# Optimization experiments

Measured on AMD Instinct MI355X. Metric: run time of the kernel, lower is better.

## Reference

```python
import jax, jax.numpy as jnp
import numpy as np

EPS = 1e-5
KH = KW = 3
PAD = 1

def conv3x3(x, w, b=None):
    out = jax.lax.conv_general_dilated(
        x, w, window_strides=(1, 1), padding=((PAD, PAD), (PAD, PAD)),
        dimension_numbers=("NCHW", "OIHW", "NCHW"))
    if b is not None:
        out = out + b[None, :, None, None]
    return out

def batchnorm(x, gamma, beta):
    # training-mode BatchNorm2d: batch statistics over (N, H, W)
    mean = x.mean(axis=(0, 2, 3), keepdims=True)
    var = x.var(axis=(0, 2, 3), keepdims=True)
    return gamma[None, :, None, None] * (x - mean) / jnp.sqrt(var + EPS) + beta[None, :, None, None]

def bilinear_gather(x, y_pos, x_pos):
    # x: [B,C,H,W]; y_pos/x_pos: [B,P,H,W] (P = KH*KW sampling taps)
    # zero padding outside image (mmcv modulated deform conv semantics)
    B, C, H, W = x.shape
    P = y_pos.shape[1]
    x_flat = x.reshape(B, C, H * W)
    y0 = jnp.floor(y_pos)
    x0 = jnp.floor(x_pos)
    ly = y_pos - y0
    lx = x_pos - x0
    out = jnp.zeros((B, C, P, H, W), dtype=x.dtype)
    for dy, dx, wgt in ((0, 0, (1 - ly) * (1 - lx)), (0, 1, (1 - ly) * lx),
                        (1, 0, ly * (1 - lx)), (1, 1, ly * lx)):
        yi = y0 + dy
        xi = x0 + dx
        valid = ((yi >= 0) & (yi <= H - 1) & (xi >= 0) & (xi <= W - 1)).astype(x.dtype)
        yc = jnp.clip(yi, 0, H - 1).astype(jnp.int32)
        xc = jnp.clip(xi, 0, W - 1).astype(jnp.int32)
        idx = (yc * W + xc).reshape(B, 1, P * H * W)
        vals = jnp.take_along_axis(x_flat, jnp.broadcast_to(idx, (B, C, P * H * W)), axis=2)
        vals = vals.reshape(B, C, P, H, W)
        out = out + vals * (wgt * valid)[:, None]
    return out  # [B,C,P,H,W]

def modulated_deform_conv(x, w_off, b_off, w_dcn):
    B, C, H, W = x.shape
    P = KH * KW
    off = conv3x3(x, w_off, b_off)  # [B, 3*P, H, W]
    o1, o2, m = jnp.split(off, 3, axis=1)
    offset = jnp.concatenate([o1, o2], axis=1)            # [B, 2P, H, W]
    offset = offset.reshape(B, P, 2, H, W)                # channel 2p -> dy, 2p+1 -> dx
    mask = jax.nn.sigmoid(m)                              # [B, P, H, W]
    hh = jnp.arange(H, dtype=x.dtype)
    ww = jnp.arange(W, dtype=x.dtype)
    ky = jnp.arange(KH, dtype=x.dtype)
    kx = jnp.arange(KW, dtype=x.dtype)
    # base sampling grid per tap p = ky*KW + kx: (h - PAD + ky, w - PAD + kx)
    base_y = (hh[None, :] - PAD + ky[:, None])            # [KH, H]
    base_x = (ww[None, :] - PAD + kx[:, None])            # [KW, W]
    base_y = jnp.broadcast_to(base_y[:, None, :, None], (KH, KW, H, W)).reshape(P, H, W)
    base_x = jnp.broadcast_to(base_x[None, :, None, :], (KH, KW, H, W)).reshape(P, H, W)
    y_pos = base_y[None] + offset[:, :, 0]                # [B,P,H,W]
    x_pos = base_x[None] + offset[:, :, 1]
    sampled = bilinear_gather(x, y_pos, x_pos)            # [B,C,P,H,W]
    sampled = sampled * mask[:, None]
    w = w_dcn.reshape(w_dcn.shape[0], C, P)               # [O, C, P]
    return jnp.einsum("bcphw,ocp->bohw", sampled, w)

def setup_inputs() -> dict:
    key = jax.random.key(0)
    ks = jax.random.split(key, 10)
    B, Ch, H, W = 4, 256, 64, 64
    Cin, Cout = 2 * Ch, 256
    P = KH * KW
    inp = {
        "input_v": jax.random.normal(ks[0], (B, Ch, H, W), jnp.float32),
        "input_i": jax.random.normal(ks[1], (B, Ch, H, W), jnp.float32),
        "w_off": jax.random.normal(ks[2], (3 * P, Cin, KH, KW), jnp.float32) * 0.01,
        "b_off": jnp.zeros((3 * P,), jnp.float32),
        "w_dcn": jax.random.normal(ks[3], (Cout, Cin, KH, KW), jnp.float32) * (1.0 / np.sqrt(Cin * P)),
        "gamma1": jnp.ones((Cout,), jnp.float32),
        "beta1": jnp.zeros((Cout,), jnp.float32),
        "w2": jax.random.normal(ks[4], (Cout, Cout, KH, KW), jnp.float32) * (1.0 / np.sqrt(Cout * P)),
        "gamma2": jnp.ones((Cout,), jnp.float32),
        "beta2": jnp.zeros((Cout,), jnp.float32),
    }
    return inp

def reference(input_v, input_i, w_off, b_off, w_dcn, gamma1, beta1, w2, gamma2, beta2):
    x = jnp.concatenate([input_v, input_i], axis=1)
    out = modulated_deform_conv(x, w_off, b_off, w_dcn)
    out = jax.nn.relu(batchnorm(out, gamma1, beta1))
    out = jax.nn.relu(batchnorm(conv3x3(out, w2), gamma2, beta2))
    return out
```

## Files before the change

### kernel.cpp

```cpp
#include <hip/hip_runtime.h>
#include <cstdint>
#include <cstddef>

typedef unsigned short u16;
typedef __attribute__((ext_vector_type(8))) short s16x8;
typedef __attribute__((ext_vector_type(4))) float f32x4;

#define DEV __device__ __forceinline__

DEV float bf2f(short u){
  union { unsigned int i; float f; } v;
  v.i = ((unsigned int)(u16)u) << 16;
  return v.f;
}
DEV short f2bf(float f){
  union { float f; unsigned int i; } v; v.f = f;
  unsigned int u = v.i;
  u += 0x7fffu + ((u >> 16) & 1u);
  return (short)(u >> 16);
}
DEV s16x8 s16x8_zero(){
  s16x8 z;
#pragma unroll
  for(int j=0;j<8;j++) z[j]=0;
  return z;
}
DEV f32x4 f32x4_zero(){
  f32x4 z;
#pragma unroll
  for(int j=0;j<4;j++) z[j]=0.f;
  return z;
}
DEV f32x4 mfma16(s16x8 a, s16x8 b, f32x4 c){
  return __builtin_amdgcn_mfma_f32_16x16x32_bf16(a, b, c, 0, 0, 0);
}
DEV void bar_lds(){
  asm volatile("s_waitcnt lgkmcnt(0)");
  __builtin_amdgcn_s_barrier();
}

static constexpr size_t OFF_ACC_B  = 0;
static constexpr size_t OUT1_ACC_B = 2097152;
static constexpr size_t OUT2_ACC_B = OUT1_ACC_B + 16777216;
static constexpr size_t STATS_B    = OUT2_ACC_B + 16777216;
static constexpr size_t ZERO_BYTES = STATS_B + 4096;
static constexpr size_t XN_B       = ZERO_BYTES;
static constexpr size_t OUT1N_B    = XN_B + 16777216;
static constexpr size_t WOFFT_B    = OUT1N_B + 8388608;
static constexpr size_t WDCNT_B    = WOFFT_B + 294912;
static constexpr size_t W2T_B      = WDCNT_B + 2359296;

__global__ void k_x_to_nhwc(const float* __restrict__ v, const float* __restrict__ vi,
                            u16* __restrict__ xn){
  __shared__ float tile[64][65];
  const int b = blockIdx.z, c0 = blockIdx.y*64, hw0 = blockIdx.x*64;
  const float* src = (c0 < 256) ? (v  + ((size_t)b*256 + c0)      *4096)
                                : (vi + ((size_t)b*256 + (c0-256))*4096);
  const int t = threadIdx.x;
#pragma unroll
  for(int k=0;k<16;k++){
    int idx = t + k*256;
    int cl = idx >> 6, wl = idx & 63;
    tile[cl][wl] = src[(size_t)cl*4096 + hw0 + wl];
  }
  __syncthreads();
#pragma unroll
  for(int k=0;k<16;k++){
    int idx = t + k*256;
    int wl = idx >> 6, cl = idx & 63;
    xn[(size_t)(b*4096 + hw0 + wl)*512 + c0 + cl] = (u16)f2bf(tile[cl][wl]);
  }
}

__global__ void k_prep_woff(const float* __restrict__ w, u16* __restrict__ wt){
  int idx = blockIdx.x*256 + threadIdx.x;
  if(idx >= 32*4608) return;
  int n = idx / 4608, k = idx % 4608;
  int t = k >> 9, c = k & 511;
  float val = (n < 27) ? w[(size_t)(n*512 + c)*9 + t] : 0.f;
  wt[idx] = (u16)f2bf(val);
}
__global__ void k_prep_wdcn(const float* __restrict__ w, u16* __restrict__ wt){
  int idx = blockIdx.x*256 + threadIdx.x;
  if(idx >= 256*4608) return;
  int n = idx / 4608, k = idx % 4608;
  int t = k >> 9, c = k & 511;
  wt[idx] = (u16)f2bf(w[(size_t)(n*512 + c)*9 + t]);
}
__global__ void k_prep_w2(const float* __restrict__ w, u16* __restrict__ wt){
  int idx = blockIdx.x*256 + threadIdx.x;
  if(idx >= 256*2304) return;
  int n = idx / 2304, k = idx % 2304;
  int t = k >> 8, c = k & 255;
  wt[idx] = (u16)f2bf(w[(size_t)(n*256 + c)*9 + t]);
}

__global__ __launch_bounds__(256, 2) void k_conv_off(
    const u16* __restrict__ xn, const u16* __restrict__ wt, float* __restrict__ offa){
  __shared__ short A_lds[4][128][8];
  __shared__ short B_lds[4][32][8];
  const int tid = threadIdx.x;
  const int lane = tid & 63, wid = tid >> 6;
  const int quad = lane >> 4, ln = lane & 15;
  const int m0 = blockIdx.x * 128;
  const int b = m0 >> 12;
  const int h0 = (m0 & 4095) >> 6;
  const int ks = blockIdx.y;
  const int ts0 = (ks == 3) ? 6 : ks*2;
  const int ntap = (ks == 3) ? 3 : 2;
  const int m_base = wid * 32;
  const int r = tid >> 1, sp = (tid & 1) * 2;
  const int h_r = h0 + (r >> 6), w_r = r & 63;
  const s16x8* Ap = (const s16x8*)A_lds;
  const s16x8* Bp = (const s16x8*)B_lds;
  f32x4 acc[2][2];
#pragma unroll
  for(int mf=0;mf<2;mf++)
#pragma unroll
    for(int nf=0;nf<2;nf++) acc[mf][nf] = f32x4_zero();

  auto load_it = [&](int it, s16x8& v0, s16x8& v1, s16x8& bv){
    const int tp = ts0 + (it >> 4);
    const int cA = (it & 15)*32;
    const int ty = tp/3, tx = tp - ty*3;
    const int y = h_r - 1 + ty, x = w_r - 1 + tx;
    const bool vld = (y>=0) & (y<64) & (x>=0) & (x<64);
    v0 = s16x8_zero(); v1 = s16x8_zero();
    if(vld){
      const u16* src = xn + ((size_t)((b<<12) + (y<<6) + x) << 9) + cA + sp*8;
      v0 = *(const s16x8*)(src);
      v1 = *(const s16x8*)(src + 8);
    }
    if(tid < 128){
      const int n = tid & 31, s2 = tid >> 5;
      bv = *(const s16x8*)(wt + (size_t)n*4608 + tp*512 + cA + s2*8);
    }
  };

  const int NIT = ntap * 16;
  s16x8 v0a, v1a, bva, v0b, v1b, bvb;
  bva = s16x8_zero(); bvb = s16x8_zero();
  load_it(0, v0a, v1a, bva);
  load_it(1, v0b, v1b, bvb);
  for(int it = 0; it < NIT; it += 2){
    bar_lds();
    *(s16x8*)(&A_lds[sp][r][0])   = v0a;
    *(s16x8*)(&A_lds[sp+1][r][0]) = v1a;
    if(tid < 128){
      const int n = tid & 31, s2 = tid >> 5;
      *(s16x8*)(&B_lds[s2][n][0]) = bva;
    }
    if(it + 2 < NIT) load_it(it + 2, v0a, v1a, bva);
    bar_lds();
    {
      s16x8 a0 = Ap[quad*128 + m_base + ln];
      s16x8 a1 = Ap[quad*128 + m_base + 16 + ln];
      s16x8 b0 = Bp[quad*32 + ln];
      s16x8 b1 = Bp[quad*32 + 16 + ln];
      acc[0][0] = mfma16(a0, b0, acc[0][0]);
      acc[0][1] = mfma16(a0, b1, acc[0][1]);
      acc[1][0] = mfma16(a1, b0, acc[1][0]);
      acc[1][1] = mfma16(a1, b1, acc[1][1]);
    }
    bar_lds();
    *(s16x8*)(&A_lds[sp][r][0])   = v0b;
    *(s16x8*)(&A_lds[sp+1][r][0]) = v1b;
    if(tid < 128){
      const int n = tid & 31, s2 = tid >> 5;
      *(s16x8*)(&B_lds[s2][n][0]) = bvb;
    }
    if(it + 3 < NIT) load_it(it + 3, v0b, v1b, bvb);
    bar_lds();
    {
      s16x8 a0 = Ap[quad*128 + m_base + ln];
      s16x8 a1 = Ap[quad*128 + m_base + 16 + ln];
      s16x8 b0 = Bp[quad*32 + ln];
      s16x8 b1 = Bp[quad*32 + 16 + ln];
      acc[0][0] = mfma16(a0, b0, acc[0][0]);
      acc[0][1] = mfma16(a0, b1, acc[0][1]);
      acc[1][0] = mfma16(a1, b0, acc[1][0]);
      acc[1][1] = mfma16(a1, b1, acc[1][1]);
    }
  }
#pragma unroll
  for(int mf=0;mf<2;mf++)
#pragma unroll
    for(int nf=0;nf<2;nf++){
      const int col = nf*16 + ln;
#pragma unroll
      for(int i=0;i<4;i++){
        const int row = m_base + mf*16 + quad*4 + i;
        unsafeAtomicAdd(offa + (size_t)(m0+row)*32 + col, acc[mf][nf][i]);
      }
    }
}

__global__ __launch_bounds__(256, 2) void k_dcn(
    const u16* __restrict__ xn, const u16* __restrict__ wt,
    const float* __restrict__ offa, const float* __restrict__ boff,
    float* __restrict__ outa){
  __shared__ short A_lds[4][64][8];
  __shared__ short B_lds[4][256][8];
  __shared__ int   p_ofs[5][4][64];
  __shared__ float p_wgt[5][4][64];
  const int tid = threadIdx.x;
  const int lane = tid & 63, wid = tid >> 6;
  const int quad = lane >> 4, ln = lane & 15;
  const int m0 = blockIdx.x * 64;
  const int b = m0 >> 12;
  const int h = (m0 & 4095) >> 6;
  const int tg = blockIdx.y;
  const int ts0 = tg ? 4 : 0;
  const int ntap = tg ? 5 : 4;
  const int wm = wid >> 1, wn = wid & 1;
  const int m_base = wm*32, n_base = wn*128;
  const int r = tid >> 2, sub = tid & 3;
  const s16x8* Ap = (const s16x8*)A_lds;
  const s16x8* Bp = (const s16x8*)B_lds;
  const u16* wrowt = wt + (size_t)tid*4608;
  f32x4 acc[2][8];
#pragma unroll
  for(int mf=0;mf<2;mf++)
#pragma unroll
    for(int nf=0;nf<8;nf++) acc[mf][nf] = f32x4_zero();

  {
    const int rr = tid & 63;
    const float* orow = offa + (size_t)(m0+rr)*32;
    for(int tpi = tid >> 6; tpi < ntap; tpi += 4){
      const int tp = ts0 + tpi;
      float dy = orow[2*tp]   + boff[2*tp];
      float dx = orow[2*tp+1] + boff[2*tp+1];
      float mz = orow[18+tp]  + boff[18+tp];
      float mk = 1.f / (1.f + expf(-mz));
      float ypos = (float)(h - 1 + tp/3) + dy;
      float xpos = (float)(rr - 1 + tp%3) + dx;
      float y0f = floorf(ypos), x0f = floorf(xpos);
      float ly = ypos - y0f, lx = xpos - x0f;
      int y0 = (int)y0f, x0 = (int)x0f;
#pragma unroll
      for(int k=0;k<4;k++){
        int ddy = k >> 1, ddx = k & 1;
        int yi = y0 + ddy, xi = x0 + ddx;
        bool vv = (yi >= 0) & (yi < 64) & (xi >= 0) & (xi < 64);
        float wk = (ddy ? ly : 1.f-ly) * (ddx ? lx : 1.f-lx) * mk;
        if(!vv) wk = 0.f;
        int yc = yi < 0 ? 0 : (yi > 63 ? 63 : yi);
        int xc = xi < 0 ? 0 : (xi > 63 ? 63 : xi);
        p_ofs[tpi][k][rr] = ((b << 12) + (yc << 6) + xc) << 9;
        p_wgt[tpi][k][rr] = wk;
      }
    }
  }
  __syncthreads();

  auto loadA = [&](int it, s16x8& a0, s16x8& a1, s16x8& a2, s16x8& a3,
                   float& w0, float& w1, float& w2, float& w3){
    const int tpi = it >> 4;
    const int c0 = (it & 15)*32 + sub*8;
    w0 = p_wgt[tpi][0][r]; w1 = p_wgt[tpi][1][r];
    w2 = p_wgt[tpi][2][r]; w3 = p_wgt[tpi][3][r];
    a0 = *(const s16x8*)(xn + p_ofs[tpi][0][r] + c0);
    a1 = *(const s16x8*)(xn + p_ofs[tpi][1][r] + c0);
    a2 = *(const s16x8*)(xn + p_ofs[tpi][2][r] + c0);
    a3 = *(const s16x8*)(xn + p_ofs[tpi][3][r] + c0);
  };
  auto loadB = [&](int it, s16x8& b0, s16x8& b1, s16x8& b2, s16x8& b3){
    const int kb = (ts0 + (it >> 4))*512 + (it & 15)*32;
    b0 = *(const s16x8*)(wrowt + kb);
    b1 = *(const s16x8*)(wrowt + kb + 8);
    b2 = *(const s16x8*)(wrowt + kb + 16);
    b3 = *(const s16x8*)(wrowt + kb + 24);
  };
  auto blend = [&](const s16x8& a0, const s16x8& a1, const s16x8& a2, const s16x8& a3,
                   float w0, float w1, float w2, float w3){
    s16x8 pk;
#pragma unroll
    for(int j=0;j<8;j++){
      float f = w0 * bf2f(a0[j]);
      f = fmaf(w1, bf2f(a1[j]), f);
      f = fmaf(w2, bf2f(a2[j]), f);
      f = fmaf(w3, bf2f(a3[j]), f);
      pk[j] = f2bf(f);
    }
    return pk;
  };

  const int NIT = ntap * 16;
  s16x8 aA0,aA1,aA2,aA3, bA0,bA1,bA2,bA3;
  s16x8 aB0,aB1,aB2,aB3, bB0,bB1,bB2,bB3;
  float wA0,wA1,wA2,wA3, wB0,wB1,wB2,wB3;
  loadA(0, aA0,aA1,aA2,aA3, wA0,wA1,wA2,wA3);
  loadB(0, bA0,bA1,bA2,bA3);
  loadA(1, aB0,aB1,aB2,aB3, wB0,wB1,wB2,wB3);
  loadB(1, bB0,bB1,bB2,bB3);

  for(int it = 0; it < NIT; it += 2){
    {
      s16x8 pk = blend(aA0,aA1,aA2,aA3, wA0,wA1,wA2,wA3);
      if(it + 2 < NIT) loadA(it + 2, aA0,aA1,aA2,aA3, wA0,wA1,wA2,wA3);
      bar_lds();
      *(s16x8*)(&A_lds[sub][r][0]) = pk;
      *(s16x8*)(&B_lds[0][tid][0]) = bA0;
      *(s16x8*)(&B_lds[1][tid][0]) = bA1;
      *(s16x8*)(&B_lds[2][tid][0]) = bA2;
      *(s16x8*)(&B_lds[3][tid][0]) = bA3;
      if(it + 2 < NIT) loadB(it + 2, bA0,bA1,bA2,bA3);
      bar_lds();
      s16x8 af0 = Ap[quad*64 + m_base + ln];
      s16x8 af1 = Ap[quad*64 + m_base + 16 + ln];
      s16x8 bfr[8];
#pragma unroll
      for(int nf=0;nf<8;nf++) bfr[nf] = Bp[quad*256 + n_base + nf*16 + ln];
#pragma unroll
      for(int nf=0;nf<8;nf++){
        acc[0][nf] = mfma16(af0, bfr[nf], acc[0][nf]);
        acc[1][nf] = mfma16(af1, bfr[nf], acc[1][nf]);
      }
    }
    {
      s16x8 pk = blend(aB0,aB1,aB2,aB3, wB0,wB1,wB2,wB3);
      if(it + 3 < NIT) loadA(it + 3, aB0,aB1,aB2,aB3, wB0,wB1,wB2,wB3);
      bar_lds();
      *(s16x8*)(&A_lds[sub][r][0]) = pk;
      *(s16x8*)(&B_lds[0][tid][0]) = bB0;
      *(s16x8*)(&B_lds[1][tid][0]) = bB1;
      *(s16x8*)(&B_lds[2][tid][0]) = bB2;
      *(s16x8*)(&B_lds[3][tid][0]) = bB3;
      if(it + 3 < NIT) loadB(it + 3, bB0,bB1,bB2,bB3);
      bar_lds();
      s16x8 af0 = Ap[quad*64 + m_base + ln];
      s16x8 af1 = Ap[quad*64 + m_base + 16 + ln];
      s16x8 bfr[8];
#pragma unroll
      for(int nf=0;nf<8;nf++) bfr[nf] = Bp[quad*256 + n_base + nf*16 + ln];
#pragma unroll
      for(int nf=0;nf<8;nf++){
        acc[0][nf] = mfma16(af0, bfr[nf], acc[0][nf]);
        acc[1][nf] = mfma16(af1, bfr[nf], acc[1][nf]);
      }
    }
  }
#pragma unroll
  for(int mf=0;mf<2;mf++)
#pragma unroll
    for(int nf=0;nf<8;nf++){
      const int col = n_base + nf*16 + ln;
#pragma unroll
      for(int i=0;i<4;i++){
        const int row = m_base + mf*16 + quad*4 + i;
        unsafeAtomicAdd(outa + (size_t)(m0+row)*256 + col, acc[mf][nf][i]);
      }
    }
}

__global__ __launch_bounds__(256, 2) void k_conv2(
    const u16* __restrict__ a_in, const u16* __restrict__ wt, float* __restrict__ outa){
  __shared__ short A_lds[4][64][8];
  __shared__ short B_lds[4][256][8];
  const int tid = threadIdx.x;
  const int lane = tid & 63, wid = tid >> 6;
  const int quad = lane >> 4, ln = lane & 15;
  const int m0 = blockIdx.x * 64;
  const int b = m0 >> 12;
  const int h = (m0 & 4095) >> 6;
  const int tg = blockIdx.y;
  const int ts0 = tg ? 4 : 0;
  const int ntap = tg ? 5 : 4;
  const int wm = wid >> 1, wn = wid & 1;
  const int m_base = wm*32, n_base = wn*128;
  const int r = tid >> 2, sub = tid & 3;
  const s16x8* Ap = (const s16x8*)A_lds;
  const s16x8* Bp = (const s16x8*)B_lds;
  const u16* wrowt = wt + (size_t)tid*2304;
  f32x4 acc[2][8];
#pragma unroll
  for(int mf=0;mf<2;mf++)
#pragma unroll
    for(int nf=0;nf<8;nf++) acc[mf][nf] = f32x4_zero();

  auto load_it = [&](int it, s16x8& va, s16x8& b0, s16x8& b1, s16x8& b2, s16x8& b3){
    const int tp = ts0 + (it >> 3);
    const int c0 = (it & 7)*32;
    const int ty = tp/3, tx = tp - ty*3;
    const int y = h - 1 + ty, x = r - 1 + tx;
    const bool vld = (y>=0) & (y<64) & (x>=0) & (x<64);
    va = s16x8_zero();
    if(vld) va = *(const s16x8*)(a_in + (((size_t)((b<<12) + (y<<6) + x)) << 8) + c0 + sub*8);
    const int kb = tp*256 + c0;
    b0 = *(const s16x8*)(wrowt + kb);
    b1 = *(const s16x8*)(wrowt + kb + 8);
    b2 = *(const s16x8*)(wrowt + kb + 16);
    b3 = *(const s16x8*)(wrowt + kb + 24);
  };

  const int NIT = ntap * 8;
  s16x8 vA, bA0,bA1,bA2,bA3;
  s16x8 vB, bB0,bB1,bB2,bB3;
  load_it(0, vA, bA0,bA1,bA2,bA3);
  load_it(1, vB, bB0,bB1,bB2,bB3);
  for(int it = 0; it < NIT; it += 2){
    bar_lds();
    *(s16x8*)(&A_lds[sub][r][0]) = vA;
    *(s16x8*)(&B_lds[0][tid][0]) = bA0;
    *(s16x8*)(&B_lds[1][tid][0]) = bA1;
    *(s16x8*)(&B_lds[2][tid][0]) = bA2;
    *(s16x8*)(&B_lds[3][tid][0]) = bA3;
    if(it + 2 < NIT) load_it(it + 2, vA, bA0,bA1,bA2,bA3);
    bar_lds();
    {
      s16x8 af0 = Ap[quad*64 + m_base + ln];
      s16x8 af1 = Ap[quad*64 + m_base + 16 + ln];
      s16x8 bfr[8];
#pragma unroll
      for(int nf=0;nf<8;nf++) bfr[nf] = Bp[quad*256 + n_base + nf*16 + ln];
#pragma unroll
      for(int nf=0;nf<8;nf++){
        acc[0][nf] = mfma16(af0, bfr[nf], acc[0][nf]);
        acc[1][nf] = mfma16(af1, bfr[nf], acc[1][nf]);
      }
    }
    bar_lds();
    *(s16x8*)(&A_lds[sub][r][0]) = vB;
    *(s16x8*)(&B_lds[0][tid][0]) = bB0;
    *(s16x8*)(&B_lds[1][tid][0]) = bB1;
    *(s16x8*)(&B_lds[2][tid][0]) = bB2;
    *(s16x8*)(&B_lds[3][tid][0]) = bB3;
    if(it + 3 < NIT) load_it(it + 3, vB, bB0,bB1,bB2,bB3);
    bar_lds();
    {
      s16x8 af0 = Ap[quad*64 + m_base + ln];
      s16x8 af1 = Ap[quad*64 + m_base + 16 + ln];
      s16x8 bfr[8];
#pragma unroll
      for(int nf=0;nf<8;nf++) bfr[nf] = Bp[quad*256 + n_base + nf*16 + ln];
#pragma unroll
      for(int nf=0;nf<8;nf++){
        acc[0][nf] = mfma16(af0, bfr[nf], acc[0][nf]);
        acc[1][nf] = mfma16(af1, bfr[nf], acc[1][nf]);
      }
    }
  }
#pragma unroll
  for(int mf=0;mf<2;mf++)
#pragma unroll
    for(int nf=0;nf<8;nf++){
      const int col = n_base + nf*16 + ln;
#pragma unroll
      for(int i=0;i<4;i++){
        const int row = m_base + mf*16 + quad*4 + i;
        unsafeAtomicAdd(outa + (size_t)(m0+row)*256 + col, acc[mf][nf][i]);
      }
    }
}

__global__ void k_stats(const float* __restrict__ acc, float* __restrict__ sum,
                        float* __restrict__ sq){
  const int m0 = blockIdx.x*64;
  const int c = threadIdx.x;
  float s = 0.f, q = 0.f;
  for(int i=0;i<64;i++){
    float v = acc[(size_t)(m0+i)*256 + c];
    s += v; q += v*v;
  }
  unsafeAtomicAdd(sum + c, s);
  unsafeAtomicAdd(sq + c, q);
}

__global__ void k_bn1(const float* __restrict__ acc, const float* __restrict__ sum,
                      const float* __restrict__ sq, const float* __restrict__ g,
                      const float* __restrict__ bt, u16* __restrict__ o){
  __shared__ float sc[256], sh[256];
  const int t = threadIdx.x;
  {
    float mean = sum[t] * (1.f/16384.f);
    float var  = sq[t] * (1.f/16384.f) - mean*mean;
    float rstd = rsqrtf(var + 1e-5f);
    float s = g[t] * rstd;
    sc[t] = s; sh[t] = bt[t] - mean*s;
  }
  __syncthreads();
  const int c4 = (t & 63) * 4;
  const float s0 = sc[c4], s1 = sc[c4+1], s2 = sc[c4+2], s3 = sc[c4+3];
  const float h0 = sh[c4], h1 = sh[c4+1], h2 = sh[c4+2], h3 = sh[c4+3];
#pragma unroll
  for(int k=0;k<4;k++){
    int m = blockIdx.x*16 + k*4 + (t>>6);
    const float4 v = *(const float4*)(acc + (size_t)m*256 + c4);
    unsigned int lo = (unsigned int)(u16)f2bf(fmaxf(0.f, v.x*s0 + h0))
                    | ((unsigned int)(u16)f2bf(fmaxf(0.f, v.y*s1 + h1)) << 16);
    unsigned int hi = (unsigned int)(u16)f2bf(fmaxf(0.f, v.z*s2 + h2))
                    | ((unsigned int)(u16)f2bf(fmaxf(0.f, v.w*s3 + h3)) << 16);
    uint2 pr; pr.x = lo; pr.y = hi;
    *(uint2*)(o + (size_t)m*256 + c4) = pr;
  }
}

__global__ void k_bn2_out(const float* __restrict__ acc, const float* __restrict__ sum,
                          const float* __restrict__ sq, const float* __restrict__ g,
                          const float* __restrict__ bt, float* __restrict__ out){
  __shared__ float tile[64][65];
  __shared__ float sc[64], sh[64];
  const int t = threadIdx.x;
  const int b = blockIdx.z, c0 = blockIdx.y*64, hw0 = blockIdx.x*64;
  if(t < 64){
    int c = c0 + t;
    float mean = sum[c] * (1.f/16384.f);
    float var  = sq[c] * (1.f/16384.f) - mean*mean;
    float rstd = rsqrtf(var + 1e-5f);
    float s = g[c] * rstd;
    sc[t] = s; sh[t] = bt[c] - mean*s;
  }
  __syncthreads();
#pragma unroll
  for(int k=0;k<16;k++){
    int idx = t + k*256;
    int wl = idx >> 6, cl = idx & 63;
    float v = acc[(size_t)((b<<12) + hw0 + wl)*256 + c0 + cl];
    tile[wl][cl] = fmaxf(0.f, v*sc[cl] + sh[cl]);
  }
  __syncthreads();
#pragma unroll
  for(int k=0;k<16;k++){
    int idx = t + k*256;
    int cl = idx >> 6, wl = idx & 63;
    out[(size_t)(b*256 + c0 + cl)*4096 + hw0 + wl] = tile[wl][cl];
  }
}

extern "C" void kernel_launch(void* const* d_in, const int* in_sizes, int n_in,
                              void* d_out, int out_size, void* d_ws, size_t ws_size,
                              hipStream_t stream){
  const float* in_v  = (const float*)d_in[0];
  const float* in_i  = (const float*)d_in[1];
  const float* w_off = (const float*)d_in[2];
  const float* b_off = (const float*)d_in[3];
  const float* w_dcn = (const float*)d_in[4];
  const float* g1    = (const float*)d_in[5];
  const float* bt1   = (const float*)d_in[6];
  const float* w2    = (const float*)d_in[7];
  const float* g2    = (const float*)d_in[8];
  const float* bt2   = (const float*)d_in[9];
  float* out = (float*)d_out;
  char* ws = (char*)d_ws;

  float* off_acc  = (float*)(ws + OFF_ACC_B);
  float* out1_acc = (float*)(ws + OUT1_ACC_B);
  float* out2_acc = (float*)(ws + OUT2_ACC_B);
  float* stats    = (float*)(ws + STATS_B);
  float* sum1 = stats,       *sq1 = stats + 256;
  float* sum2 = stats + 512, *sq2 = stats + 768;
  u16* xn    = (u16*)(ws + XN_B);
  u16* out1n = (u16*)(ws + OUT1N_B);
  u16* wofft = (u16*)(ws + WOFFT_B);
  u16* wdcnt = (u16*)(ws + WDCNT_B);
  u16* w2t   = (u16*)(ws + W2T_B);

  hipMemsetAsync(ws, 0, ZERO_BYTES, stream);
  k_x_to_nhwc<<<dim3(64,8,4), 256, 0, stream>>>(in_v, in_i, xn);
  k_prep_woff<<<576, 256, 0, stream>>>(w_off, wofft);
  k_prep_wdcn<<<4608, 256, 0, stream>>>(w_dcn, wdcnt);
  k_prep_w2<<<2304, 256, 0, stream>>>(w2, w2t);
  k_conv_off<<<dim3(128,4), 256, 0, stream>>>(xn, wofft, off_acc);
  k_dcn<<<dim3(256,2), 256, 0, stream>>>(xn, wdcnt, off_acc, b_off, out1_acc);
  k_stats<<<256, 256, 0, stream>>>(out1_acc, sum1, sq1);
  k_bn1<<<1024, 256, 0, stream>>>(out1_acc, sum1, sq1, g1, bt1, out1n);
  k_conv2<<<dim3(256,2), 256, 0, stream>>>(out1n, w2t, out2_acc);
  k_stats<<<256, 256, 0, stream>>>(out2_acc, sum2, sq2);
  k_bn2_out<<<dim3(64,4,4), 256, 0, stream>>>(out2_acc, sum2, sq2, g2, bt2, out);
}
```

Baseline: 352.0 us.

## Enlarge DCN and conv2 GEMM tiles to 128x256 with 512-thread blocks

Both implicit-GEMM kernels (deformable conv and second conv) move from 64-row, 256-thread blocks to 128-row, 512-thread blocks with a 2x4 wave grid, each wave computing a 64x64 sub-tile (4x4 MFMA fragments). The K step per barrier pair doubles to 64 channels, so each weight row is loaded once per 128 output pixels instead of 64, and each barrier covers twice the MFMA work. The intent is to halve weight traffic and reduce barrier and LDS overhead per FLOP. The cost is higher register pressure (16 accumulators plus double-buffered gather registers in the DCN kernel), more LDS per block, and half as many blocks (256 per kernel), which may reduce occupancy and load balance.

```diff
diff --git a/kernel.cpp b/kernel.cpp
--- a/kernel.cpp
+++ b/kernel.cpp
@@ -195,46 +195,48 @@
     }
 }
 
-__global__ __launch_bounds__(256, 2) void k_dcn(
+__global__ __launch_bounds__(512, 2) void k_dcn(
     const u16* __restrict__ xn, const u16* __restrict__ wt,
     const float* __restrict__ offa, const float* __restrict__ boff,
     float* __restrict__ outa){
-  __shared__ short A_lds[4][64][8];
-  __shared__ short B_lds[4][256][8];
-  __shared__ int   p_ofs[5][4][64];
-  __shared__ float p_wgt[5][4][64];
+  __shared__ short A_lds[8][128][8];
+  __shared__ short B_lds[8][256][8];
+  __shared__ int   p_ofs[5][4][128];
+  __shared__ float p_wgt[5][4][128];
   const int tid = threadIdx.x;
-  const int lane = tid & 63, wid = tid >> 6;
+  const int lane = tid & 63;
   const int quad = lane >> 4, ln = lane & 15;
-  const int m0 = blockIdx.x * 64;
+  const int wid = tid >> 6;
+  const int wm = wid >> 2, wn = wid & 3;
+  const int m0 = blockIdx.x * 128;
   const int b = m0 >> 12;
-  const int h = (m0 & 4095) >> 6;
+  const int h0 = (m0 & 4095) >> 6;
   const int tg = blockIdx.y;
   const int ts0 = tg ? 4 : 0;
   const int ntap = tg ? 5 : 4;
-  const int wm = wid >> 1, wn = wid & 1;
-  const int m_base = wm*32, n_base = wn*128;
-  const int r = tid >> 2, sub = tid & 3;
+  const int r_s = tid >> 2, sub = tid & 3;
+  const int nB = tid & 255, hB = tid >> 8;
   const s16x8* Ap = (const s16x8*)A_lds;
   const s16x8* Bp = (const s16x8*)B_lds;
-  const u16* wrowt = wt + (size_t)tid*4608;
-  f32x4 acc[2][8];
-#pragma unroll
-  for(int mf=0;mf<2;mf++)
-#pragma unroll
-    for(int nf=0;nf<8;nf++) acc[mf][nf] = f32x4_zero();
+  const u16* wrowB = wt + (size_t)nB*4608 + hB*32;
+  f32x4 acc[4][4];
+#pragma unroll
+  for(int mf=0;mf<4;mf++)
+#pragma unroll
+    for(int nf=0;nf<4;nf++) acc[mf][nf] = f32x4_zero();
 
   {
-    const int rr = tid & 63;
+    const int rr = tid & 127;
+    const int h_rr = h0 + (rr >> 6), w_rr = rr & 63;
     const float* orow = offa + (size_t)(m0+rr)*32;
-    for(int tpi = tid >> 6; tpi < ntap; tpi += 4){
+    for(int tpi = tid >> 7; tpi < ntap; tpi += 4){
       const int tp = ts0 + tpi;
       float dy = orow[2*tp]   + boff[2*tp];
       float dx = orow[2*tp+1] + boff[2*tp+1];
       float mz = orow[18+tp]  + boff[18+tp];
       float mk = 1.f / (1.f + expf(-mz));
-      float ypos = (float)(h - 1 + tp/3) + dy;
-      float xpos = (float)(rr - 1 + tp%3) + dx;
+      float ypos = (float)(h_rr - 1 + tp/3) + dy;
+      float xpos = (float)(w_rr - 1 + tp%3) + dx;
       float y0f = floorf(ypos), x0f = floorf(xpos);
       float ly = ypos - y0f, lx = xpos - x0f;
       int y0 = (int)y0f, x0 = (int)x0f;
@@ -254,26 +256,31 @@
   }
   __syncthreads();
 
-  auto loadA = [&](int it, s16x8& a0, s16x8& a1, s16x8& a2, s16x8& a3,
+  auto loadA = [&](int p, s16x8& a00, s16x8& a01, s16x8& a10, s16x8& a11,
+                   s16x8& a20, s16x8& a21, s16x8& a30, s16x8& a31,
                    float& w0, float& w1, float& w2, float& w3){
-    const int tpi = it >> 4;
-    const int c0 = (it & 15)*32 + sub*8;
-    w0 = p_wgt[tpi][0][r]; w1 = p_wgt[tpi][1][r];
-    w2 = p_wgt[tpi][2][r]; w3 = p_wgt[tpi][3][r];
-    a0 = *(const s16x8*)(xn + p_ofs[tpi][0][r] + c0);
-    a1 = *(const s16x8*)(xn + p_ofs[tpi][1][r] + c0);
-    a2 = *(const s16x8*)(xn + p_ofs[tpi][2][r] + c0);
-    a3 = *(const s16x8*)(xn + p_ofs[tpi][3][r] + c0);
-  };
-  auto loadB = [&](int it, s16x8& b0, s16x8& b1, s16x8& b2, s16x8& b3){
-    const int kb = (ts0 + (it >> 4))*512 + (it & 15)*32;
-    b0 = *(const s16x8*)(wrowt + kb);
-    b1 = *(const s16x8*)(wrowt + kb + 8);
-    b2 = *(const s16x8*)(wrowt + kb + 16);
-    b3 = *(const s16x8*)(wrowt + kb + 24);
-  };
-  auto blend = [&](const s16x8& a0, const s16x8& a1, const s16x8& a2, const s16x8& a3,
-                   float w0, float w1, float w2, float w3){
+    const int tpi = p >> 3;
+    const int c0 = (p & 7)*64 + sub*8;
+    w0 = p_wgt[tpi][0][r_s]; w1 = p_wgt[tpi][1][r_s];
+    w2 = p_wgt[tpi][2][r_s]; w3 = p_wgt[tpi][3][r_s];
+    const u16* s0 = xn + p_ofs[tpi][0][r_s] + c0;
+    const u16* s1 = xn + p_ofs[tpi][1][r_s] + c0;
+    const u16* s2 = xn + p_ofs[tpi][2][r_s] + c0;
+    const u16* s3 = xn + p_ofs[tpi][3][r_s] + c0;
+    a00 = *(const s16x8*)(s0);  a01 = *(const s16x8*)(s0 + 32);
+    a10 = *(const s16x8*)(s1);  a11 = *(const s16x8*)(s1 + 32);
+    a20 = *(const s16x8*)(s2);  a21 = *(const s16x8*)(s2 + 32);
+    a30 = *(const s16x8*)(s3);  a31 = *(const s16x8*)(s3 + 32);
+  };
+  auto loadB = [&](int p, s16x8& b0, s16x8& b1, s16x8& b2, s16x8& b3){
+    const u16* src = wrowB + (ts0 + (p >> 3))*512 + (p & 7)*64;
+    b0 = *(const s16x8*)(src);
+    b1 = *(const s16x8*)(src + 8);
+    b2 = *(const s16x8*)(src + 16);
+    b3 = *(const s16x8*)(src + 24);
+  };
+  auto blend2 = [&](const s16x8& a0, const s16x8& a1, const s16x8& a2, const s16x8& a3,
+                    float w0, float w1, float w2, float w3){
     s16x8 pk;
 #pragma unroll
     for(int j=0;j<8;j++){
@@ -285,170 +292,173 @@
     }
     return pk;
   };
-
-  const int NIT = ntap * 16;
-  s16x8 aA0,aA1,aA2,aA3, bA0,bA1,bA2,bA3;
-  s16x8 aB0,aB1,aB2,aB3, bB0,bB1,bB2,bB3;
-  float wA0,wA1,wA2,wA3, wB0,wB1,wB2,wB3;
-  loadA(0, aA0,aA1,aA2,aA3, wA0,wA1,wA2,wA3);
-  loadB(0, bA0,bA1,bA2,bA3);
-  loadA(1, aB0,aB1,aB2,aB3, wB0,wB1,wB2,wB3);
-  loadB(1, bB0,bB1,bB2,bB3);
-
-  for(int it = 0; it < NIT; it += 2){
+  auto mfma_phase = [&](){
+#pragma unroll
+    for(int kk=0;kk<2;kk++){
+      s16x8 af[4], bf[4];
+#pragma unroll
+      for(int mf=0;mf<4;mf++) af[mf] = Ap[(kk*4+quad)*128 + wm*64 + mf*16 + ln];
+#pragma unroll
+      for(int nf=0;nf<4;nf++) bf[nf] = Bp[(kk*4+quad)*256 + wn*64 + nf*16 + ln];
+#pragma unroll
+      for(int mf=0;mf<4;mf++)
+#pragma unroll
+        for(int nf=0;nf<4;nf++) acc[mf][nf] = mfma16(af[mf], bf[nf], acc[mf][nf]);
+    }
+  };
+
+  const int NP = ntap * 8;
+  s16x8 xA00,xA01,xA10,xA11,xA20,xA21,xA30,xA31, yA00,yA01,yA10,yA11,yA20,yA21,yA30,yA31;
+  s16x8 xB0,xB1,xB2,xB3, yB0,yB1,yB2,yB3;
+  float xw0,xw1,xw2,xw3, yw0,yw1,yw2,yw3;
+  loadA(0, xA00,xA01,xA10,xA11,xA20,xA21,xA30,xA31, xw0,xw1,xw2,xw3);
+  loadB(0, xB0,xB1,xB2,xB3);
+  loadA(1, yA00,yA01,yA10,yA11,yA20,yA21,yA30,yA31, yw0,yw1,yw2,yw3);
+  loadB(1, yB0,yB1,yB2,yB3);
+
+  for(int p = 0; p < NP; p += 2){
     {
-      s16x8 pk = blend(aA0,aA1,aA2,aA3, wA0,wA1,wA2,wA3);
-      if(it + 2 < NIT) loadA(it + 2, aA0,aA1,aA2,aA3, wA0,wA1,wA2,wA3);
+      s16x8 pk0 = blend2(xA00,xA10,xA20,xA30, xw0,xw1,xw2,xw3);
+      s16x8 pk1 = blend2(xA01,xA11,xA21,xA31, xw0,xw1,xw2,xw3);
+      if(p + 2 < NP) loadA(p + 2, xA00,xA01,xA10,xA11,xA20,xA21,xA30,xA31, xw0,xw1,xw2,xw3);
       bar_lds();
-      *(s16x8*)(&A_lds[sub][r][0]) = pk;
-      *(s16x8*)(&B_lds[0][tid][0]) = bA0;
-      *(s16x8*)(&B_lds[1][tid][0]) = bA1;
-      *(s16x8*)(&B_lds[2][tid][0]) = bA2;
-      *(s16x8*)(&B_lds[3][tid][0]) = bA3;
-      if(it + 2 < NIT) loadB(it + 2, bA0,bA1,bA2,bA3);
+      *(s16x8*)(&A_lds[sub][r_s][0])     = pk0;
+      *(s16x8*)(&A_lds[4+sub][r_s][0])   = pk1;
+      *(s16x8*)(&B_lds[hB*4+0][nB][0]) = xB0;
+      *(s16x8*)(&B_lds[hB*4+1][nB][0]) = xB1;
+      *(s16x8*)(&B_lds[hB*4+2][nB][0]) = xB2;
+      *(s16x8*)(&B_lds[hB*4+3][nB][0]) = xB3;
+      if(p + 2 < NP) loadB(p + 2, xB0,xB1,xB2,xB3);
       bar_lds();
-      s16x8 af0 = Ap[quad*64 + m_base + ln];
-      s16x8 af1 = Ap[quad*64 + m_base + 16 + ln];
-      s16x8 bfr[8];
-#pragma unroll
-      for(int nf=0;nf<8;nf++) bfr[nf] = Bp[quad*256 + n_base + nf*16 + ln];
-#pragma unroll
-      for(int nf=0;nf<8;nf++){
-        acc[0][nf] = mfma16(af0, bfr[nf], acc[0][nf]);
-        acc[1][nf] = mfma16(af1, bfr[nf], acc[1][nf]);
-      }
+      mfma_phase();
     }
     {
-      s16x8 pk = blend(aB0,aB1,aB2,aB3, wB0,wB1,wB2,wB3);
-      if(it + 3 < NIT) loadA(it + 3, aB0,aB1,aB2,aB3, wB0,wB1,wB2,wB3);
+      s16x8 pk0 = blend2(yA00,yA10,yA20,yA30, yw0,yw1,yw2,yw3);
+      s16x8 pk1 = blend2(yA01,yA11,yA21,yA31, yw0,yw1,yw2,yw3);
+      if(p + 3 < NP) loadA(p + 3, yA00,yA01,yA10,yA11,yA20,yA21,yA30,yA31, yw0,yw1,yw2,yw3);
       bar_lds();
-      *(s16x8*)(&A_lds[sub][r][0]) = pk;
-      *(s16x8*)(&B_lds[0][tid][0]) = bB0;
-      *(s16x8*)(&B_lds[1][tid][0]) = bB1;
-      *(s16x8*)(&B_lds[2][tid][0]) = bB2;
-      *(s16x8*)(&B_lds[3][tid][0]) = bB3;
-      if(it + 3 < NIT) loadB(it + 3, bB0,bB1,bB2,bB3);
+      *(s16x8*)(&A_lds[sub][r_s][0])     = pk0;
+      *(s16x8*)(&A_lds[4+sub][r_s][0])   = pk1;
+      *(s16x8*)(&B_lds[hB*4+0][nB][0]) = yB0;
+      *(s16x8*)(&B_lds[hB*4+1][nB][0]) = yB1;
+      *(s16x8*)(&B_lds[hB*4+2][nB][0]) = yB2;
+      *(s16x8*)(&B_lds[hB*4+3][nB][0]) = yB3;
+      if(p + 3 < NP) loadB(p + 3, yB0,yB1,yB2,yB3);
       bar_lds();
-      s16x8 af0 = Ap[quad*64 + m_base + ln];
-      s16x8 af1 = Ap[quad*64 + m_base + 16 + ln];
-      s16x8 bfr[8];
-#pragma unroll
-      for(int nf=0;nf<8;nf++) bfr[nf] = Bp[quad*256 + n_base + nf*16 + ln];
-#pragma unroll
-      for(int nf=0;nf<8;nf++){
-        acc[0][nf] = mfma16(af0, bfr[nf], acc[0][nf]);
-        acc[1][nf] = mfma16(af1, bfr[nf], acc[1][nf]);
-      }
-    }
-  }
-#pragma unroll
-  for(int mf=0;mf<2;mf++)
-#pragma unroll
-    for(int nf=0;nf<8;nf++){
-      const int col = n_base + nf*16 + ln;
+      mfma_phase();
+    }
+  }
+#pragma unroll
+  for(int mf=0;mf<4;mf++)
+#pragma unroll
+    for(int nf=0;nf<4;nf++){
+      const int col = wn*64 + nf*16 + ln;
 #pragma unroll
       for(int i=0;i<4;i++){
-        const int row = m_base + mf*16 + quad*4 + i;
+        const int row = wm*64 + mf*16 + quad*4 + i;
         unsafeAtomicAdd(outa + (size_t)(m0+row)*256 + col, acc[mf][nf][i]);
       }
     }
 }
 
-__global__ __launch_bounds__(256, 2) void k_conv2(
+__global__ __launch_bounds__(512, 2) void k_conv2(
     const u16* __restrict__ a_in, const u16* __restrict__ wt, float* __restrict__ outa){
-  __shared__ short A_lds[4][64][8];
-  __shared__ short B_lds[4][256][8];
+  __shared__ short A_lds[8][128][8];
+  __shared__ short B_lds[8][256][8];
   const int tid = threadIdx.x;
-  const int lane = tid & 63, wid = tid >> 6;
+  const int lane = tid & 63;
   const int quad = lane >> 4, ln = lane & 15;
-  const int m0 = blockIdx.x * 64;
+  const int wid = tid >> 6;
+  const int wm = wid >> 2, wn = wid & 3;
+  const int m0 = blockIdx.x * 128;
   const int b = m0 >> 12;
-  const int h = (m0 & 4095) >> 6;
+  const int h0 = (m0 & 4095) >> 6;
   const int tg = blockIdx.y;
   const int ts0 = tg ? 4 : 0;
   const int ntap = tg ? 5 : 4;
-  const int wm = wid >> 1, wn = wid & 1;
-  const int m_base = wm*32, n_base = wn*128;
-  const int r = tid >> 2, sub = tid & 3;
+  const int r_s = tid >> 2, sub = tid & 3;
+  const int nB = tid & 255, hB = tid >> 8;
+  const int h_rs = h0 + (r_s >> 6), w_rs = r_s & 63;
   const s16x8* Ap = (const s16x8*)A_lds;
   const s16x8* Bp = (const s16x8*)B_lds;
-  const u16* wrowt = wt + (size_t)tid*2304;
-  f32x4 acc[2][8];
-#pragma unroll
-  for(int mf=0;mf<2;mf++)
-#pragma unroll
-    for(int nf=0;nf<8;nf++) acc[mf][nf] = f32x4_zero();
-
-  auto load_it = [&](int it, s16x8& va, s16x8& b0, s16x8& b1, s16x8& b2, s16x8& b3){
-    const int tp = ts0 + (it >> 3);
-    const int c0 = (it & 7)*32;
+  const u16* wrowB = wt + (size_t)nB*2304 + hB*32;
+  f32x4 acc[4][4];
+#pragma unroll
+  for(int mf=0;mf<4;mf++)
+#pragma unroll
+    for(int nf=0;nf<4;nf++) acc[mf][nf] = f32x4_zero();
+
+  auto loadA = [&](int p, s16x8& a0, s16x8& a1){
+    const int tp = ts0 + (p >> 2);
+    const int c0 = (p & 3)*64 + sub*8;
     const int ty = tp/3, tx = tp - ty*3;
-    const int y = h - 1 + ty, x = r - 1 + tx;
+    const int y = h_rs - 1 + ty, x = w_rs - 1 + tx;
     const bool vld = (y>=0) & (y<64) & (x>=0) & (x<64);
-    va = s16x8_zero();
-    if(vld) va = *(const s16x8*)(a_in + (((size_t)((b<<12) + (y<<6) + x)) << 8) + c0 + sub*8);
-    const int kb = tp*256 + c0;
-    b0 = *(const s16x8*)(wrowt + kb);
-    b1 = *(const s16x8*)(wrowt + kb + 8);
-    b2 = *(const s16x8*)(wrowt + kb + 16);
-    b3 = *(const s16x8*)(wrowt + kb + 24);
-  };
-
-  const int NIT = ntap * 8;
-  s16x8 vA, bA0,bA1,bA2,bA3;
-  s16x8 vB, bB0,bB1,bB2,bB3;
-  load_it(0, vA, bA0,bA1,bA2,bA3);
-  load_it(1, vB, bB0,bB1,bB2,bB3);
-  for(int it = 0; it < NIT; it += 2){
-    bar_lds();
-    *(s16x8*)(&A_lds[sub][r][0]) = vA;
-    *(s16x8*)(&B_lds[0][tid][0]) = bA0;
-    *(s16x8*)(&B_lds[1][tid][0]) = bA1;
-    *(s16x8*)(&B_lds[2][tid][0]) = bA2;
-    *(s16x8*)(&B_lds[3][tid][0]) = bA3;
-    if(it + 2 < NIT) load_it(it + 2, vA, bA0,bA1,bA2,bA3);
-    bar_lds();
-    {
-      s16x8 af0 = Ap[quad*64 + m_base + ln];
-      s16x8 af1 = Ap[quad*64 + m_base + 16 + ln];
-      s16x8 bfr[8];
-#pragma unroll
-      for(int nf=0;nf<8;nf++) bfr[nf] = Bp[quad*256 + n_base + nf*16 + ln];
-#pragma unroll
-      for(int nf=0;nf<8;nf++){
-        acc[0][nf] = mfma16(af0, bfr[nf], acc[0][nf]);
-        acc[1][nf] = mfma16(af1, bfr[nf], acc[1][nf]);
-      }
-    }
-    bar_lds();
-    *(s16x8*)(&A_lds[sub][r][0]) = vB;
-    *(s16x8*)(&B_lds[0][tid][0]) = bB0;
-    *(s16x8*)(&B_lds[1][tid][0]) = bB1;
-    *(s16x8*)(&B_lds[2][tid][0]) = bB2;
-    *(s16x8*)(&B_lds[3][tid][0]) = bB3;
-    if(it + 3 < NIT) load_it(it + 3, vB, bB0,bB1,bB2,bB3);
-    bar_lds();
-    {
-      s16x8 af0 = Ap[quad*64 + m_base + ln];
-      s16x8 af1 = Ap[quad*64 + m_base + 16 + ln];
-      s16x8 bfr[8];
-#pragma unroll
-      for(int nf=0;nf<8;nf++) bfr[nf] = Bp[quad*256 + n_base + nf*16 + ln];
-#pragma unroll
-      for(int nf=0;nf<8;nf++){
-        acc[0][nf] = mfma16(af0, bfr[nf], acc[0][nf]);
-        acc[1][nf] = mfma16(af1, bfr[nf], acc[1][nf]);
-      }
-    }
-  }
-#pragma unroll
-  for(int mf=0;mf<2;mf++)
-#pragma unroll
-    for(int nf=0;nf<8;nf++){
-      const int col = n_base + nf*16 + ln;
+    a0 = s16x8_zero(); a1 = s16x8_zero();
+    if(vld){
+      const u16* src = a_in + (((size_t)((b<<12) + (y<<6) + x)) << 8) + c0;
+      a0 = *(const s16x8*)(src);
+      a1 = *(const s16x8*)(src + 32);
+    }
+  };
+  auto loadB = [&](int p, s16x8& b0, s16x8& b1, s16x8& b2, s16x8& b3){
+    const u16* src = wrowB + (ts0 + (p >> 2))*256 + (p & 3)*64;
+    b0 = *(const s16x8*)(src);
+    b1 = *(const s16x8*)(src + 8);
+    b2 = *(const s16x8*)(src + 16);
+    b3 = *(const s16x8*)(src + 24);
+  };
+  auto mfma_phase = [&](){
+#pragma unroll
+    for(int kk=0;kk<2;kk++){
+      s16x8 af[4], bf[4];
+#pragma unroll
+      for(int mf=0;mf<4;mf++) af[mf] = Ap[(kk*4+quad)*128 + wm*64 + mf*16 + ln];
+#pragma unroll
+      for(int nf=0;nf<4;nf++) bf[nf] = Bp[(kk*4+quad)*256 + wn*64 + nf*16 + ln];
+#pragma unroll
+      for(int mf=0;mf<4;mf++)
+#pragma unroll
+        for(int nf=0;nf<4;nf++) acc[mf][nf] = mfma16(af[mf], bf[nf], acc[mf][nf]);
+    }
+  };
+
+  const int NP = ntap * 4;
+  s16x8 xA0,xA1, xB0,xB1,xB2,xB3;
+  s16x8 yA0,yA1, yB0,yB1,yB2,yB3;
+  loadA(0, xA0,xA1); loadB(0, xB0,xB1,xB2,xB3);
+  loadA(1, yA0,yA1); loadB(1, yB0,yB1,yB2,yB3);
+
+  for(int p = 0; p < NP; p += 2){
+    bar_lds();
+    *(s16x8*)(&A_lds[sub][r_s][0])   = xA0;
+    *(s16x8*)(&A_lds[4+sub][r_s][0]) = xA1;
+    *(s16x8*)(&B_lds[hB*4+0][nB][0]) = xB0;
+    *(s16x8*)(&B_lds[hB*4+1][nB][0]) = xB1;
+    *(s16x8*)(&B_lds[hB*4+2][nB][0]) = xB2;
+    *(s16x8*)(&B_lds[hB*4+3][nB][0]) = xB3;
+    if(p + 2 < NP){ loadA(p + 2, xA0,xA1); loadB(p + 2, xB0,xB1,xB2,xB3); }
+    bar_lds();
+    mfma_phase();
+    bar_lds();
+    *(s16x8*)(&A_lds[sub][r_s][0])   = yA0;
+    *(s16x8*)(&A_lds[4+sub][r_s][0]) = yA1;
+    *(s16x8*)(&B_lds[hB*4+0][nB][0]) = yB0;
+    *(s16x8*)(&B_lds[hB*4+1][nB][0]) = yB1;
+    *(s16x8*)(&B_lds[hB*4+2][nB][0]) = yB2;
+    *(s16x8*)(&B_lds[hB*4+3][nB][0]) = yB3;
+    if(p + 3 < NP){ loadA(p + 3, yA0,yA1); loadB(p + 3, yB0,yB1,yB2,yB3); }
+    bar_lds();
+    mfma_phase();
+  }
+#pragma unroll
+  for(int mf=0;mf<4;mf++)
+#pragma unroll
+    for(int nf=0;nf<4;nf++){
+      const int col = wn*64 + nf*16 + ln;
 #pragma unroll
       for(int i=0;i<4;i++){
-        const int row = m_base + mf*16 + quad*4 + i;
+        const int row = wm*64 + mf*16 + quad*4 + i;
         unsafeAtomicAdd(outa + (size_t)(m0+row)*256 + col, acc[mf][nf][i]);
       }
     }
@@ -562,10 +572,10 @@
   k_prep_wdcn<<<4608, 256, 0, stream>>>(w_dcn, wdcnt);
   k_prep_w2<<<2304, 256, 0, stream>>>(w2, w2t);
   k_conv_off<<<dim3(128,4), 256, 0, stream>>>(xn, wofft, off_acc);
-  k_dcn<<<dim3(256,2), 256, 0, stream>>>(xn, wdcnt, off_acc, b_off, out1_acc);
+  k_dcn<<<dim3(128,2), 512, 0, stream>>>(xn, wdcnt, off_acc, b_off, out1_acc);
   k_stats<<<256, 256, 0, stream>>>(out1_acc, sum1, sq1);
   k_bn1<<<1024, 256, 0, stream>>>(out1_acc, sum1, sq1, g1, bt1, out1n);
-  k_conv2<<<dim3(256,2), 256, 0, stream>>>(out1n, w2t, out2_acc);
+  k_conv2<<<dim3(128,2), 512, 0, stream>>>(out1n, w2t, out2_acc);
   k_stats<<<256, 256, 0, stream>>>(out2_acc, sum2, sq2);
   k_bn2_out<<<dim3(64,4,4), 256, 0, stream>>>(out2_acc, sum2, sq2, g2, bt2, out);
 }
```

New measurement: 350.3 us. Within noise of the previous version (-0.5%).
